# Performance work log

Hardware: AMD Instinct MI355X
Metric: run time of the kernel (lower is better)

Reference implementation:

```python
import jax, jax.numpy as jnp
import numpy as np

IN_C, OUT_C, K, STRIDE, PAD, N_EXPERTS = 64, 128, 3, 1, 1, 4
B, H, W = 32, 64, 64


def setup_inputs() -> dict:
    key = jax.random.key(0)
    k1, k2, k3, k4 = jax.random.split(key, 4)
    x = jax.random.normal(k1, (B, IN_C, H, W), dtype=jnp.float32)
    idx = jax.random.randint(k2, (B,), 0, N_EXPERTS, dtype=jnp.int64)
    # Expert conv weights/biases (PyTorch Conv2d layout: [out_c, in_c, kh, kw])
    fan_in = IN_C * K * K
    bound = 1.0 / np.sqrt(fan_in)
    Wc = jax.random.uniform(k3, (N_EXPERTS, OUT_C, IN_C, K, K), dtype=jnp.float32,
                            minval=-bound, maxval=bound)
    bc = jax.random.uniform(k4, (N_EXPERTS, OUT_C), dtype=jnp.float32,
                            minval=-bound, maxval=bound)
    return {"x": x, "idx": idx, "Wc": Wc, "bc": bc}


def _conv2d(x, w, b):
    # x: [B, C_in, H, W], w: [C_out, C_in, K, K], b: [C_out]
    y = jax.lax.conv_general_dilated(
        x, w,
        window_strides=(STRIDE, STRIDE),
        padding=[(PAD, PAD), (PAD, PAD)],
        dimension_numbers=("NCHW", "OIHW", "NCHW"),
    )
    return y + b[None, :, None, None]


def reference(x, idx, Wc, bc):
    # Compute every expert's conv for every sample (faithful to the torch code),
    # then gather each sample's selected expert output.
    results = jax.vmap(lambda w, b: _conv2d(x, w, b))(Wc, bc)  # [E, B, C_out, H, W]
    results = jnp.moveaxis(results, 0, 1)                      # [B, E, C_out, H, W]
    out = jnp.take_along_axis(
        results, idx[:, None, None, None, None].astype(jnp.int32), axis=1
    )  # [B, 1, C_out, H, W]
    return jnp.squeeze(out, axis=1)
```

## Files before the change

kernel.cpp:

```cpp
#include <hip/hip_runtime.h>
#include <hip/hip_bf16.h>


#define IC 64
#define OC 128
#define HH 64
#define WW 64

typedef short short8 __attribute__((ext_vector_type(8)));
typedef float float16 __attribute__((ext_vector_type(16)));

static __device__ __forceinline__ ushort f2bf(float v) {
    __hip_bfloat16 h = __float2bfloat16(v);
    return *(ushort*)&h;
}

__global__ __launch_bounds__(256)
void reorder_w(const float* __restrict__ Wc, ushort* __restrict__ wout) {
    const int blk = blockIdx.x;
    const int e   = blk / 9;
    const int tap = blk - e * 9;
    const float* __restrict__ src = Wc + (size_t)e * OC * IC * 9 + tap;
    ushort2* __restrict__ dst = (ushort2*)(wout + (size_t)blk * 8192);
    for (int j = threadIdx.x; j < 4096; j += 256) {
        const int ich = j >> 9;
        const int oc  = (j >> 2) & 127;
        const int ip  = j & 3;
        const int ic  = ich * 8 + ip * 2;
        const float v0 = src[(oc * IC + ic) * 9];
        const float v1 = src[(oc * IC + ic + 1) * 9];
        ushort2 u;
        u.x = f2bf(v0);
        u.y = f2bf(v1);
        dst[j] = u;
    }
}

__global__ __launch_bounds__(512)
void moe_conv_mfma(const float* __restrict__ x, const int* __restrict__ idx,
                   const ushort* __restrict__ wre, const float* __restrict__ bc,
                   float* __restrict__ out) {
    __shared__ __align__(16) ushort xs[6 * 8 * 66 * 8];
    __shared__ __align__(16) ushort wlds[8192];
    __shared__ float bias[128];

    const int t    = threadIdx.x;
    const int rq   = blockIdx.x;
    const int b    = blockIdx.y;
    const int row0 = rq * 4;
    const int e    = ((unsigned)idx[b]) & 3;

    if (t < 192) {
        const int r = t >> 5, rem = t & 31;
        const int ich = rem >> 2, side = (rem >> 1) & 1, q = rem & 1;
        const int hc = side ? 65 : 0;
        ushort4 z = {0, 0, 0, 0};
        *(ushort4*)&xs[(((r * 8 + ich) * 66 + hc) * 8 + q * 4)] = z;
    } else if (t < 320) {
        bias[t - 192] = bc[e * OC + (t - 192)];
    }

    const float* xb = x + (size_t)b * IC * HH * WW;
    {
        const int gc   = t & 63;
        const int csel = t >> 6;
#pragma unroll
        for (int it = 0; it < 12; ++it) {
            const int combo = it * 8 + csel;
            const int r = combo >> 4, rem = combo & 15;
            const int ich = rem >> 1, q = rem & 1;
            const int gr = row0 - 1 + r;
            ushort4 u = {0, 0, 0, 0};
            if ((unsigned)gr < (unsigned)HH) {
                const int ic0 = ich * 8 + q * 4;
                u.x = f2bf(xb[((ic0 + 0) * HH + gr) * WW + gc]);
                u.y = f2bf(xb[((ic0 + 1) * HH + gr) * WW + gc]);
                u.z = f2bf(xb[((ic0 + 2) * HH + gr) * WW + gc]);
                u.w = f2bf(xb[((ic0 + 3) * HH + gr) * WW + gc]);
            }
            *(ushort4*)&xs[(((r * 8 + ich) * 66 + (gc + 1)) * 8 + q * 4)] = u;
        }
    }

    const int lane31 = t & 31;
    const int lhi    = (t >> 5) & 1;
    const int wv     = t >> 6;
    const int w0     = wv & 1;
    const int pr     = wv >> 1;

    float16 acc[2][2];
#pragma unroll
    for (int a = 0; a < 2; ++a)
#pragma unroll
        for (int cg = 0; cg < 2; ++cg)
#pragma unroll
            for (int r = 0; r < 16; ++r) acc[a][cg][r] = 0.0f;

    const ushort* wsrc = wre + (size_t)e * 9 * 8192;

    for (int tap = 0; tap < 9; ++tap) {
        __syncthreads();
        {
            const ushort* g0 = wsrc + tap * 8192;
#pragma unroll
            for (int i = 0; i < 2; ++i) {
                const int g = i * 512 + t;
                __builtin_amdgcn_global_load_lds(
                    (const __attribute__((address_space(1))) unsigned int*)(g0 + g * 8),
                    (__attribute__((address_space(3))) unsigned int*)&wlds[g * 8],
                    16, 0, 0);
            }
        }
        __syncthreads();

        const int kh = tap / 3;
        const int kw = tap - kh * 3;
        const int rr = pr + kh;
        const int hb = lane31 + kw;

#pragma unroll
        for (int ks = 0; ks < 4; ++ks) {
            const int ich = ks * 2 + lhi;
            const short8 a0 = *(const short8*)&wlds[(ich * 128 + w0 * 64 + lane31) * 8];
            const short8 a1 = *(const short8*)&wlds[(ich * 128 + w0 * 64 + 32 + lane31) * 8];
            const short8 b0 = *(const short8*)&xs[((rr * 8 + ich) * 66 + hb) * 8];
            const short8 b1 = *(const short8*)&xs[((rr * 8 + ich) * 66 + hb + 32) * 8];
            acc[0][0] = __builtin_amdgcn_mfma_f32_32x32x16_bf16(a0, b0, acc[0][0], 0, 0, 0);
            acc[0][1] = __builtin_amdgcn_mfma_f32_32x32x16_bf16(a0, b1, acc[0][1], 0, 0, 0);
            acc[1][0] = __builtin_amdgcn_mfma_f32_32x32x16_bf16(a1, b0, acc[1][0], 0, 0, 0);
            acc[1][1] = __builtin_amdgcn_mfma_f32_32x32x16_bf16(a1, b1, acc[1][1], 0, 0, 0);
        }
    }

#pragma unroll
    for (int a = 0; a < 2; ++a) {
        const int ocb = w0 * 64 + a * 32 + 4 * lhi;
#pragma unroll
        for (int reg = 0; reg < 16; ++reg) {
            const int oc = ocb + (reg & 3) + 8 * (reg >> 2);
            const float bv = bias[oc];
            const size_t base = (((size_t)b * OC + oc) * HH + (row0 + pr)) * WW;
            out[base + lane31]      = acc[a][0][reg] + bv;
            out[base + 32 + lane31] = acc[a][1][reg] + bv;
        }
    }
}

extern "C" void kernel_launch(void* const* d_in, const int* in_sizes, int n_in,
                              void* d_out, int out_size, void* d_ws, size_t ws_size,
                              hipStream_t stream) {
    const float* x   = (const float*)d_in[0];
    const int*   idx = (const int*)d_in[1];
    const float* Wc  = (const float*)d_in[2];
    const float* bc  = (const float*)d_in[3];
    float* out  = (float*)d_out;
    ushort* wre = (ushort*)d_ws;

    reorder_w<<<36, 256, 0, stream>>>(Wc, wre);
    dim3 grid(16, 32);
    moe_conv_mfma<<<grid, 512, 0, stream>>>(x, idx, wre, bc, out);
}
```

Measured before the change: 114.6 us.

## Prefetch next tap weights into registers and parallelize weight reorder kernel

The weight reorder kernel now uses one thread per source element across 1152 blocks, reading coalesced and scattering bf16 writes, replacing 36 blocks with strided gathers. The conv kernel replaces the direct global-to-LDS load per tap with a register prefetch of the next tap's weights, issued after the barrier so it overlaps the MFMA work of the current tap. This costs extra VGPRs per thread, which may reduce occupancy, and stores into LDS go through registers.

Result: faster. 110.3 us (-3.7%).

```diff
diff --git a/kernel.cpp b/kernel.cpp
--- a/kernel.cpp
+++ b/kernel.cpp
@@ -17,23 +17,16 @@
 
 __global__ __launch_bounds__(256)
 void reorder_w(const float* __restrict__ Wc, ushort* __restrict__ wout) {
-    const int blk = blockIdx.x;
-    const int e   = blk / 9;
-    const int tap = blk - e * 9;
-    const float* __restrict__ src = Wc + (size_t)e * OC * IC * 9 + tap;
-    ushort2* __restrict__ dst = (ushort2*)(wout + (size_t)blk * 8192);
-    for (int j = threadIdx.x; j < 4096; j += 256) {
-        const int ich = j >> 9;
-        const int oc  = (j >> 2) & 127;
-        const int ip  = j & 3;
-        const int ic  = ich * 8 + ip * 2;
-        const float v0 = src[(oc * IC + ic) * 9];
-        const float v1 = src[(oc * IC + ic + 1) * 9];
-        ushort2 u;
-        u.x = f2bf(v0);
-        u.y = f2bf(v1);
-        dst[j] = u;
-    }
+    const int n = blockIdx.x * 256 + threadIdx.x;
+    const float v = Wc[n];
+    const int e  = n / 73728;
+    int r        = n - e * 73728;
+    const int oc = r / 576;
+    r           -= oc * 576;
+    const int ic  = r / 9;
+    const int tap = r - ic * 9;
+    wout[((((size_t)e * 9 + tap) * 8 + (ic >> 3)) * 128 + oc) * 8 + (ic & 7)] =
+        f2bf(v);
 }
 
 __global__ __launch_bounds__(512)
@@ -98,20 +91,23 @@
 
     const ushort* wsrc = wre + (size_t)e * 9 * 8192;
 
+    uint4 wreg0, wreg1;
+    {
+        const uint4* g = (const uint4*)wsrc;
+        wreg0 = g[t];
+        wreg1 = g[512 + t];
+    }
+
     for (int tap = 0; tap < 9; ++tap) {
         __syncthreads();
-        {
-            const ushort* g0 = wsrc + tap * 8192;
-#pragma unroll
-            for (int i = 0; i < 2; ++i) {
-                const int g = i * 512 + t;
-                __builtin_amdgcn_global_load_lds(
-                    (const __attribute__((address_space(1))) unsigned int*)(g0 + g * 8),
-                    (__attribute__((address_space(3))) unsigned int*)&wlds[g * 8],
-                    16, 0, 0);
-            }
+        *(uint4*)&wlds[(size_t)t * 8]         = wreg0;
+        *(uint4*)&wlds[(size_t)(512 + t) * 8] = wreg1;
+        __syncthreads();
+        if (tap < 8) {
+            const uint4* g = (const uint4*)(wsrc + (tap + 1) * 8192);
+            wreg0 = g[t];
+            wreg1 = g[512 + t];
         }
-        __syncthreads();
 
         const int kh = tap / 3;
         const int kw = tap - kh * 3;
@@ -156,7 +152,7 @@
     float* out  = (float*)d_out;
     ushort* wre = (ushort*)d_ws;
 
-    reorder_w<<<36, 256, 0, stream>>>(Wc, wre);
+    reorder_w<<<1152, 256, 0, stream>>>(Wc, wre);
     dim3 grid(16, 32);
     moe_conv_mfma<<<grid, 512, 0, stream>>>(x, idx, wre, bc, out);
 }
```
